# Kernel tuning notes

Hardware: AMD Instinct MI355X
Metric: run time of the kernel (lower is better)

## Reference

```python
import jax, jax.numpy as jnp
import numpy as np

ATOMF_LEN = 82
EDGE_DIM = 6
HIDDEN = 10
GNN_DEPTH = 2
N_NODES = 200000
N_EDGES = 6400000


def _lrelu(x):
    return jax.nn.leaky_relu(x, negative_slope=0.1)


def setup_inputs() -> dict:
    key = jax.random.key(0)
    ks = jax.random.split(key, 7)
    vertex = jax.random.normal(ks[0], (N_NODES, ATOMF_LEN), dtype=jnp.float32)
    edge_feat = jax.random.normal(ks[1], (N_EDGES, EDGE_DIM), dtype=jnp.float32)
    src = jax.random.randint(ks[2], (N_EDGES,), 0, N_NODES, dtype=jnp.int32)
    dst = jax.random.randint(ks[3], (N_EDGES,), 0, N_NODES, dtype=jnp.int32)
    # kaiming-uniform-ish init scale (fan_in based)
    weight_init = jax.random.uniform(ks[4], (ATOMF_LEN, HIDDEN), dtype=jnp.float32,
                                     minval=-1.0, maxval=1.0) * (np.sqrt(6.0 / ATOMF_LEN))
    gather_weight = jax.random.uniform(ks[5], (HIDDEN + EDGE_DIM, HIDDEN), dtype=jnp.float32,
                                       minval=-1.0, maxval=1.0) * (np.sqrt(6.0 / (HIDDEN + EDGE_DIM)))
    update_weight = jax.random.uniform(ks[6], (2 * HIDDEN, HIDDEN), dtype=jnp.float32,
                                       minval=-1.0, maxval=1.0) * (np.sqrt(6.0 / (2 * HIDDEN)))
    return {"vertex": vertex, "edge_feat": edge_feat, "src": src, "dst": dst,
            "weight_init": weight_init, "gather_weight": gather_weight,
            "update_weight": update_weight}


def reference(vertex, edge_feat, src, dst, weight_init, gather_weight, update_weight):
    # embedding_: leaky_relu(mm(x, W), 0.1)
    h = _lrelu(vertex @ weight_init)  # [N, HIDDEN]
    n_nodes = vertex.shape[0]
    for _ in range(GNN_DEPTH):
        # gather: per-edge message from source node hidden + edge features
        msg = _lrelu(jnp.concatenate([h[src], edge_feat], axis=1) @ gather_weight)  # [E, HIDDEN]
        # scatter-sum aggregation onto destination nodes
        agg = jax.ops.segment_sum(msg, dst, num_segments=n_nodes)  # [N, HIDDEN]
        # update: combine current hidden with aggregated messages
        h = _lrelu(jnp.concatenate([h, agg], axis=1) @ update_weight)  # [N, HIDDEN]
    return h
```

## Files before the change

### kernel.cpp

```cpp
#include <hip/hip_runtime.h>

#define ATOMF 82
#define EDGE_DIM 6
#define HIDDEN 10
#define ZPAD 16

#define BSHIFT 8
#define BUCKN (1 << BSHIFT)
#define MAXBUCK 1024
#define NB2 256
#define MAXE3 16384

__device__ __forceinline__ float lrelu(float x) { return x > 0.f ? x : 0.1f * x; }

__device__ __forceinline__ unsigned int f2bf(float f) {
    unsigned int u = __float_as_uint(f);
    return (u + 0x7fffu + ((u >> 16) & 1u)) >> 16;
}
__device__ __forceinline__ float bf2f(unsigned int b) {
    return __uint_as_float(b << 16);
}

typedef float vf2 __attribute__((ext_vector_type(2)));
__device__ __forceinline__ int nt_i(const int* p) { return __builtin_nontemporal_load(p); }
__device__ __forceinline__ vf2 nt_f2(const float* p) {
    return __builtin_nontemporal_load((const vf2*)p);
}

__global__ void embed_kernel(const float* __restrict__ vertex,
                             const float* __restrict__ W,
                             const float* __restrict__ GW,
                             float* __restrict__ h, unsigned short* __restrict__ z,
                             int n_nodes) {
    __shared__ float w[ATOMF * HIDDEN];
    __shared__ float gwh[HIDDEN * HIDDEN];
    for (int i = threadIdx.x; i < ATOMF * HIDDEN; i += blockDim.x) w[i] = W[i];
    for (int i = threadIdx.x; i < HIDDEN * HIDDEN; i += blockDim.x) gwh[i] = GW[i];
    __syncthreads();
    int node = blockIdx.x * blockDim.x + threadIdx.x;
    if (node >= n_nodes) return;
    const float2* v = (const float2*)(vertex + (long)node * ATOMF);
    float acc[HIDDEN];
#pragma unroll
    for (int j = 0; j < HIDDEN; j++) acc[j] = 0.f;
#pragma unroll 2
    for (int k2 = 0; k2 < ATOMF / 2; k2++) {
        float2 t = v[k2];
#pragma unroll
        for (int j = 0; j < HIDDEN; j++) acc[j] += t.x * w[(2 * k2) * HIDDEN + j];
#pragma unroll
        for (int j = 0; j < HIDDEN; j++) acc[j] += t.y * w[(2 * k2 + 1) * HIDDEN + j];
    }
    float ho[HIDDEN];
    float* out = h + (long)node * HIDDEN;
#pragma unroll
    for (int j = 0; j < HIDDEN; j++) { ho[j] = lrelu(acc[j]); out[j] = ho[j]; }
    float zv[HIDDEN];
#pragma unroll
    for (int j = 0; j < HIDDEN; j++) zv[j] = 0.f;
#pragma unroll
    for (int k = 0; k < HIDDEN; k++) {
        float x = ho[k];
#pragma unroll
        for (int j = 0; j < HIDDEN; j++) zv[j] += x * gwh[k * HIDDEN + j];
    }
    unsigned int* zq = (unsigned int*)(z + (size_t)node * ZPAD);
    int4 pk;
    pk.x = (int)(f2bf(zv[0]) | (f2bf(zv[1]) << 16));
    pk.y = (int)(f2bf(zv[2]) | (f2bf(zv[3]) << 16));
    pk.z = (int)(f2bf(zv[4]) | (f2bf(zv[5]) << 16));
    pk.w = (int)(f2bf(zv[6]) | (f2bf(zv[7]) << 16));
    *(int4*)zq = pk;
    zq[4] = f2bf(zv[8]) | (f2bf(zv[9]) << 16);
}

__global__ __launch_bounds__(1024) void hist_kernel(const int* __restrict__ dst,
                                                    int* __restrict__ hist,
                                                    long n_edges, int nbuck) {
    __shared__ int hl[MAXBUCK];
    for (int t = threadIdx.x; t < nbuck; t += 1024) hl[t] = 0;
    __syncthreads();
    long per = (n_edges + gridDim.x - 1) / gridDim.x;
    long s = (long)blockIdx.x * per;
    long e = s + per; if (e > n_edges) e = n_edges;
    for (long i = s + threadIdx.x; i < e; i += 1024)
        atomicAdd(&hl[nt_i(dst + i) >> BSHIFT], 1);
    __syncthreads();
    for (int t = threadIdx.x; t < nbuck; t += 1024)
        hist[(size_t)t * gridDim.x + blockIdx.x] = hl[t];
}

__global__ __launch_bounds__(1024) void scan_block_sums(const int* __restrict__ in,
                                                        int* __restrict__ partials, int n) {
    __shared__ int ws[16];
    int i = blockIdx.x * 1024 + threadIdx.x;
    int v = (i < n) ? in[i] : 0;
    int lane = threadIdx.x & 63, wid = threadIdx.x >> 6;
    int s = v;
#pragma unroll
    for (int off = 32; off > 0; off >>= 1) s += __shfl_down(s, off, 64);
    if (lane == 0) ws[wid] = s;
    __syncthreads();
    if (threadIdx.x == 0) {
        int t = 0;
#pragma unroll
        for (int k = 0; k < 16; k++) t += ws[k];
        partials[blockIdx.x] = t;
    }
}
__global__ __launch_bounds__(1024) void scan_partials(int* __restrict__ partials, int nb) {
    __shared__ int wsum[16];
    int lane = threadIdx.x & 63, wid = threadIdx.x >> 6;
    int v = (threadIdx.x < nb) ? partials[threadIdx.x] : 0;
    int incl = v;
#pragma unroll
    for (int off = 1; off < 64; off <<= 1) {
        int t = __shfl_up(incl, off, 64);
        if (lane >= off) incl += t;
    }
    if (lane == 63) wsum[wid] = incl;
    __syncthreads();
    if (wid == 0 && lane < 16) {
        int wv = wsum[lane];
        int wincl = wv;
#pragma unroll
        for (int off = 1; off < 16; off <<= 1) {
            int t = __shfl_up(wincl, off, 64);
            if (lane >= off) wincl += t;
        }
        wsum[lane] = wincl - wv;
    }
    __syncthreads();
    if (threadIdx.x < nb) partials[threadIdx.x] = wsum[wid] + (incl - v);
}
__global__ __launch_bounds__(1024) void scan_final(const int* __restrict__ in,
                                                   const int* __restrict__ partials,
                                                   int* __restrict__ out, int n) {
    __shared__ int wsum[16];
    int i = blockIdx.x * 1024 + threadIdx.x;
    int v = (i < n) ? in[i] : 0;
    int lane = threadIdx.x & 63, wid = threadIdx.x >> 6;
    int incl = v;
#pragma unroll
    for (int off = 1; off < 64; off <<= 1) {
        int t = __shfl_up(incl, off, 64);
        if (lane >= off) incl += t;
    }
    if (lane == 63) wsum[wid] = incl;
    __syncthreads();
    if (wid == 0 && lane < 16) {
        int wv = wsum[lane];
        int wincl = wv;
#pragma unroll
        for (int off = 1; off < 16; off <<= 1) {
            int t = __shfl_up(wincl, off, 64);
            if (lane >= off) wincl += t;
        }
        wsum[lane] = wincl - wv;
    }
    __syncthreads();
    if (i <= n) out[i] = partials[blockIdx.x] + wsum[wid] + (incl - v);
}

__global__ __launch_bounds__(1024) void part_scatter_kernel(
    const int* __restrict__ src, const int* __restrict__ dst,
    const float* __restrict__ ef, const int* __restrict__ base,
    int4* __restrict__ rec, long n_edges, int nbuck) {
    __shared__ int cur[MAXBUCK];
    for (int t = threadIdx.x; t < nbuck; t += 1024)
        cur[t] = base[(size_t)t * gridDim.x + blockIdx.x];
    __syncthreads();
    long per = (n_edges + gridDim.x - 1) / gridDim.x;
    long s = (long)blockIdx.x * per;
    long e = s + per; if (e > n_edges) e = n_edges;
    for (long i = s + threadIdx.x; i < e; i += 1024) {
        int d = nt_i(dst + i);
        int slot = atomicAdd(&cur[d >> BSHIFT], 1);
        const float* ep = ef + i * (long)EDGE_DIM;
        vf2 fa = nt_f2(ep), fb = nt_f2(ep + 2), fc = nt_f2(ep + 4);
        int4 r;
        r.x = nt_i(src + i) | ((d & (BUCKN - 1)) << 24);
        r.y = (int)(f2bf(fa.x) | (f2bf(fa.y) << 16));
        r.z = (int)(f2bf(fb.x) | (f2bf(fb.y) << 16));
        r.w = (int)(f2bf(fc.x) | (f2bf(fc.y) << 16));
        rec[slot] = r;
    }
}

__global__ __launch_bounds__(512) void bucket_csr_kernel(
    const int* __restrict__ base, const int4* __restrict__ rec_a, int4* __restrict__ rec_b,
    int* __restrict__ offsets, int n_nodes) {
    __shared__ unsigned char lid[MAXE3];
    __shared__ int cnt[BUCKN];
    __shared__ int excl_s[BUCKN];
    __shared__ int cursor[BUCKN];
    int b = blockIdx.x;
    int S = base[(size_t)b * NB2];
    int E = base[(size_t)(b + 1) * NB2];
    int node0 = b << BSHIFT;
    int nn = n_nodes - node0; if (nn > BUCKN) nn = BUCKN;
    if ((int)threadIdx.x < BUCKN) cnt[threadIdx.x] = 0;
    __syncthreads();
    int ne = E - S;
    bool fit = (ne <= MAXE3);
    for (int i = threadIdx.x; i < ne; i += 512) {
        int l = (int)((unsigned int)rec_a[S + i].x >> 24);
        if (fit) lid[i] = (unsigned char)l;
        atomicAdd(&cnt[l], 1);
    }
    __syncthreads();
    if (threadIdx.x == 0) {
        int run = 0;
#pragma unroll 4
        for (int l = 0; l < BUCKN; l++) { excl_s[l] = run; run += cnt[l]; }
    }
    __syncthreads();
    if ((int)threadIdx.x < nn) offsets[node0 + threadIdx.x] = S + excl_s[threadIdx.x];
    if ((int)threadIdx.x < BUCKN) cursor[threadIdx.x] = excl_s[threadIdx.x];
    if (b == (int)gridDim.x - 1 && threadIdx.x == 0) offsets[n_nodes] = E;
    __syncthreads();
    for (int i = threadIdx.x; i < ne; i += 512) {
        int4 r = rec_a[S + i];
        int l = fit ? (int)lid[i] : (int)((unsigned int)r.x >> 24);
        int q = atomicAdd(&cursor[l], 1);
        rec_b[S + q] = r;
    }
}

__global__ void count_pos_kernel(const int* __restrict__ dst, int* __restrict__ counts,
                                 unsigned short* __restrict__ pos, long n_edges) {
    long e0 = ((long)blockIdx.x * blockDim.x + threadIdx.x) * 4;
    if (e0 + 3 < n_edges) {
        int4 d = *(const int4*)(dst + e0);
        ushort4 p;
        p.x = (unsigned short)atomicAdd(&counts[d.x], 1);
        p.y = (unsigned short)atomicAdd(&counts[d.y], 1);
        p.z = (unsigned short)atomicAdd(&counts[d.z], 1);
        p.w = (unsigned short)atomicAdd(&counts[d.w], 1);
        *(ushort4*)(pos + e0) = p;
    } else {
        for (long e = e0; e < n_edges; e++)
            pos[e] = (unsigned short)atomicAdd(&counts[dst[e]], 1);
    }
}
__global__ void scatter_rec_kernel(const int* __restrict__ src, const int* __restrict__ dst,
                                   const float* __restrict__ ef,
                                   const unsigned short* __restrict__ pos,
                                   const int* __restrict__ offsets,
                                   int4* __restrict__ rec, long n_edges) {
    long e = (long)blockIdx.x * blockDim.x + threadIdx.x;
    if (e >= n_edges) return;
    int d = dst[e];
    int q = offsets[d] + (int)pos[e];
    const float2* er = (const float2*)(ef + e * (long)EDGE_DIM);
    float2 fa = er[0], fb = er[1], fc = er[2];
    int4 r;
    r.x = src[e];
    r.y = (int)(f2bf(fa.x) | (f2bf(fa.y) << 16));
    r.z = (int)(f2bf(fb.x) | (f2bf(fb.y) << 16));
    r.w = (int)(f2bf(fc.x) | (f2bf(fc.y) << 16));
    rec[q] = r;
}

__global__ __launch_bounds__(256) void gather_update_kernel(
    const float* __restrict__ h_in, const unsigned short* __restrict__ z_in,
    const int4* __restrict__ rec, const int* __restrict__ offsets,
    const float* __restrict__ GW, const float* __restrict__ UW,
    float* __restrict__ h_out, unsigned short* __restrict__ z_out,
    int n_nodes, int write_z, unsigned int src_mask) {
    __shared__ float gwh[HIDDEN * HIDDEN];
    __shared__ float gwe[EDGE_DIM * HIDDEN];
    __shared__ float uw[2 * HIDDEN * HIDDEN];
    for (int i = threadIdx.x; i < HIDDEN * HIDDEN; i += 256) gwh[i] = GW[i];
    for (int i = threadIdx.x; i < EDGE_DIM * HIDDEN; i += 256) gwe[i] = GW[HIDDEN * HIDDEN + i];
    for (int i = threadIdx.x; i < 2 * HIDDEN * HIDDEN; i += 256) uw[i] = UW[i];
    __syncthreads();
    int group = threadIdx.x >> 4;
    int sub = threadIdx.x & 15;
    int node = blockIdx.x * 16 + group;
    if (node >= n_nodes) return;
    int off0 = offsets[node], off1 = offsets[node + 1];
    float acc[HIDDEN];
#pragma unroll
    for (int j = 0; j < HIDDEN; j++) acc[j] = 0.f;
    int p = off0 + sub;
    int4 r;
    if (p < off1) r = rec[p];
    while (p < off1) {
        int pn = p + 16;
        int4 rn = r;
        if (pn < off1) rn = rec[pn];
        int sn = (int)((unsigned int)r.x & src_mask);
        const int* zq = (const int*)(z_in + (size_t)sn * ZPAD);
        int4 za = *(const int4*)zq;
        int zb = zq[4];
        float ef[EDGE_DIM];
        unsigned int u0 = (unsigned int)r.y, u1 = (unsigned int)r.z, u2 = (unsigned int)r.w;
        ef[0] = bf2f(u0 & 0xffffu); ef[1] = bf2f(u0 >> 16);
        ef[2] = bf2f(u1 & 0xffffu); ef[3] = bf2f(u1 >> 16);
        ef[4] = bf2f(u2 & 0xffffu); ef[5] = bf2f(u2 >> 16);
        float m[HIDDEN];
#pragma unroll
        for (int j = 0; j < HIDDEN; j++) m[j] = 0.f;
#pragma unroll
        for (int k = 0; k < EDGE_DIM; k++) {
            float x = ef[k];
#pragma unroll
            for (int j = 0; j < HIDDEN; j++) m[j] += x * gwe[k * HIDDEN + j];
        }
        unsigned int z0 = (unsigned int)za.x, z1 = (unsigned int)za.y;
        unsigned int z2 = (unsigned int)za.z, z3 = (unsigned int)za.w, z4 = (unsigned int)zb;
        acc[0] += lrelu(m[0] + bf2f(z0 & 0xffffu));
        acc[1] += lrelu(m[1] + bf2f(z0 >> 16));
        acc[2] += lrelu(m[2] + bf2f(z1 & 0xffffu));
        acc[3] += lrelu(m[3] + bf2f(z1 >> 16));
        acc[4] += lrelu(m[4] + bf2f(z2 & 0xffffu));
        acc[5] += lrelu(m[5] + bf2f(z2 >> 16));
        acc[6] += lrelu(m[6] + bf2f(z3 & 0xffffu));
        acc[7] += lrelu(m[7] + bf2f(z3 >> 16));
        acc[8] += lrelu(m[8] + bf2f(z4 & 0xffffu));
        acc[9] += lrelu(m[9] + bf2f(z4 >> 16));
        r = rn; p = pn;
    }
#pragma unroll
    for (int j = 0; j < HIDDEN; j++) {
#pragma unroll
        for (int d = 8; d > 0; d >>= 1) acc[j] += __shfl_down(acc[j], d, 16);
    }
    if (sub == 0) {
        float in[2 * HIDDEN];
        const float2* hp = (const float2*)(h_in + (long)node * HIDDEN);
#pragma unroll
        for (int k = 0; k < 5; k++) { float2 t = hp[k]; in[2 * k] = t.x; in[2 * k + 1] = t.y; }
#pragma unroll
        for (int j = 0; j < HIDDEN; j++) in[HIDDEN + j] = acc[j];
        float o[HIDDEN];
#pragma unroll
        for (int j = 0; j < HIDDEN; j++) o[j] = 0.f;
#pragma unroll
        for (int k = 0; k < 2 * HIDDEN; k++) {
            float x = in[k];
#pragma unroll
            for (int j = 0; j < HIDDEN; j++) o[j] += x * uw[k * HIDDEN + j];
        }
        float ho[HIDDEN];
        float* outp = h_out + (long)node * HIDDEN;
#pragma unroll
        for (int j = 0; j < HIDDEN; j++) { ho[j] = lrelu(o[j]); outp[j] = ho[j]; }
        if (write_z) {
            float zv[HIDDEN];
#pragma unroll
            for (int j = 0; j < HIDDEN; j++) zv[j] = 0.f;
#pragma unroll
            for (int k = 0; k < HIDDEN; k++) {
                float x = ho[k];
#pragma unroll
                for (int j = 0; j < HIDDEN; j++) zv[j] += x * gwh[k * HIDDEN + j];
            }
            unsigned int* zq = (unsigned int*)(z_out + (size_t)node * ZPAD);
            int4 pk;
            pk.x = (int)(f2bf(zv[0]) | (f2bf(zv[1]) << 16));
            pk.y = (int)(f2bf(zv[2]) | (f2bf(zv[3]) << 16));
            pk.z = (int)(f2bf(zv[4]) | (f2bf(zv[5]) << 16));
            pk.w = (int)(f2bf(zv[6]) | (f2bf(zv[7]) << 16));
            *(int4*)zq = pk;
            zq[4] = f2bf(zv[8]) | (f2bf(zv[9]) << 16);
        }
    }
}

extern "C" void kernel_launch(void* const* d_in, const int* in_sizes, int n_in,
                              void* d_out, int out_size, void* d_ws, size_t ws_size,
                              hipStream_t stream) {
    const float* vertex    = (const float*)d_in[0];
    const float* edge_feat = (const float*)d_in[1];
    const int*   src       = (const int*)d_in[2];
    const int*   dst       = (const int*)d_in[3];
    const float* w_init    = (const float*)d_in[4];
    const float* gw        = (const float*)d_in[5];
    const float* uw        = (const float*)d_in[6];

    const int  n_nodes = in_sizes[0] / ATOMF;
    const long n_edges = (long)in_sizes[2];
    float* out = (float*)d_out;

    const int TB = 256;
    const int node_blocks = (n_nodes + TB - 1) / TB;
    const int gu_blocks   = (n_nodes + 15) / 16;

    const int nbuck = (n_nodes + BUCKN - 1) >> BSHIFT;
    const long m = (long)nbuck * NB2;
    const int scanb_m = (int)((m + 1 + 1023) / 1024);

    size_t tbl_bytes = (size_t)n_nodes * (2 * HIDDEN * sizeof(float) + 2 * ZPAD * sizeof(unsigned short));
    size_t rec_bytes = (size_t)n_edges * sizeof(int4);

    auto al = [](size_t x) { return (x + 255) & ~(size_t)255; };
    size_t need_new = al(m * 4) + al((m + 1) * 4) + al(2048 * 4) +
                      al((size_t)(n_nodes + 1) * 4) + al(rec_bytes) +
                      al(rec_bytes > tbl_bytes ? rec_bytes : tbl_bytes);

    char* ws = (char*)d_ws;
    size_t o = 0;
    auto alloc = [&](size_t bytes) { char* p = ws + o; o = (o + bytes + 255) & ~(size_t)255; return p; };

    if (nbuck <= MAXBUCK && scanb_m <= 1024 && n_nodes <= (1 << 24) && ws_size >= need_new) {
        int*  hist     = (int*)alloc(m * 4);
        int*  base     = (int*)alloc((m + 1) * 4);
        int*  partials = (int*)alloc(2048 * 4);
        int*  offsets  = (int*)alloc((size_t)(n_nodes + 1) * 4);
        int4* rec_b    = (int4*)alloc(rec_bytes);
        char* ovl      = alloc(rec_bytes > tbl_bytes ? rec_bytes : tbl_bytes);
        int4* rec_a    = (int4*)ovl;
        float*          h0 = (float*)ovl;
        float*          h1 = h0 + (size_t)n_nodes * HIDDEN;
        unsigned short* z0 = (unsigned short*)(h1 + (size_t)n_nodes * HIDDEN);
        unsigned short* z1 = z0 + (size_t)n_nodes * ZPAD;

        hist_kernel<<<NB2, 1024, 0, stream>>>(dst, hist, n_edges, nbuck);
        scan_block_sums<<<scanb_m, 1024, 0, stream>>>(hist, partials, (int)m);
        scan_partials<<<1, 1024, 0, stream>>>(partials, scanb_m);
        scan_final<<<scanb_m, 1024, 0, stream>>>(hist, partials, base, (int)m);
        part_scatter_kernel<<<NB2, 1024, 0, stream>>>(src, dst, edge_feat, base, rec_a,
                                                      n_edges, nbuck);
        bucket_csr_kernel<<<nbuck, 512, 0, stream>>>(base, rec_a, rec_b, offsets, n_nodes);

        embed_kernel<<<node_blocks, TB, 0, stream>>>(vertex, w_init, gw, h0, z0, n_nodes);
        gather_update_kernel<<<gu_blocks, TB, 0, stream>>>(h0, z0, rec_b, offsets, gw, uw,
                                                           h1, z1, n_nodes, 1, 0x00ffffffu);
        gather_update_kernel<<<gu_blocks, TB, 0, stream>>>(h1, z1, rec_b, offsets, gw, uw,
                                                           out, z0, n_nodes, 0, 0x00ffffffu);
    } else {
        int*  counts   = (int*)alloc((size_t)(n_nodes + 1) * 4);
        int*  offsets  = (int*)alloc((size_t)(n_nodes + 1) * 4);
        int*  partials = (int*)alloc(2048 * 4);
        int4* rec      = (int4*)alloc(rec_bytes);
        size_t pos_bytes = (size_t)n_edges * sizeof(unsigned short);
        char* overlay = alloc(pos_bytes > tbl_bytes ? pos_bytes : tbl_bytes);
        unsigned short* pos = (unsigned short*)overlay;
        float*          h0  = (float*)overlay;
        float*          h1  = h0 + (size_t)n_nodes * HIDDEN;
        unsigned short* z0  = (unsigned short*)(h1 + (size_t)n_nodes * HIDDEN);
        unsigned short* z1  = z0 + (size_t)n_nodes * ZPAD;

        const int edge_blocks = (int)((n_edges + TB - 1) / TB);
        const int cp_blocks   = (int)((n_edges / 4 + TB - 1) / TB);
        const int scan_blocks = (n_nodes + 1 + 1023) / 1024;

        hipMemsetAsync(counts, 0, (size_t)(n_nodes + 1) * 4, stream);
        count_pos_kernel<<<cp_blocks, TB, 0, stream>>>(dst, counts, pos, n_edges);
        scan_block_sums<<<scan_blocks, 1024, 0, stream>>>(counts, partials, n_nodes);
        scan_partials<<<1, 1024, 0, stream>>>(partials, scan_blocks);
        scan_final<<<scan_blocks, 1024, 0, stream>>>(counts, partials, offsets, n_nodes);
        scatter_rec_kernel<<<edge_blocks, TB, 0, stream>>>(src, dst, edge_feat, pos, offsets,
                                                           rec, n_edges);
        embed_kernel<<<node_blocks, TB, 0, stream>>>(vertex, w_init, gw, h0, z0, n_nodes);
        gather_update_kernel<<<gu_blocks, TB, 0, stream>>>(h0, z0, rec, offsets, gw, uw,
                                                           h1, z1, n_nodes, 1, 0xffffffffu);
        gather_update_kernel<<<gu_blocks, TB, 0, stream>>>(h1, z1, rec, offsets, gw, uw,
                                                           out, z0, n_nodes, 0, 0xffffffffu);
    }
    (void)ws_size;
}
```

Before: 732.2 us.

## Store local bucket ids in a separate ushort array and widen buckets to 512 nodes

Local destination ids are no longer packed into the high byte of the src field. They go into a separate 16-bit side array, which bucket_csr reads in both passes in place of reloading the 16-byte records or caching ids in shared memory. Buckets grow to 512 nodes and the partition kernel uses 512 blocks, so there are half as many buckets, each with more edges. This adds 2 bytes per edge of extra write and read traffic. It also removes the src mask from the gather kernel.

```diff
diff --git a/kernel.cpp b/kernel.cpp
--- a/kernel.cpp
+++ b/kernel.cpp
@@ -5,11 +5,10 @@
 #define HIDDEN 10
 #define ZPAD 16
 
-#define BSHIFT 8
+#define BSHIFT 9
 #define BUCKN (1 << BSHIFT)
-#define MAXBUCK 1024
-#define NB2 256
-#define MAXE3 16384
+#define MAXBUCK 512
+#define NB2 512
 
 __device__ __forceinline__ float lrelu(float x) { return x > 0.f ? x : 0.1f * x; }
 
@@ -165,7 +164,8 @@
 __global__ __launch_bounds__(1024) void part_scatter_kernel(
     const int* __restrict__ src, const int* __restrict__ dst,
     const float* __restrict__ ef, const int* __restrict__ base,
-    int4* __restrict__ rec, long n_edges, int nbuck) {
+    int4* __restrict__ rec, unsigned short* __restrict__ lid16,
+    long n_edges, int nbuck) {
     __shared__ int cur[MAXBUCK];
     for (int t = threadIdx.x; t < nbuck; t += 1024)
         cur[t] = base[(size_t)t * gridDim.x + blockIdx.x];
@@ -179,18 +179,19 @@
         const float* ep = ef + i * (long)EDGE_DIM;
         vf2 fa = nt_f2(ep), fb = nt_f2(ep + 2), fc = nt_f2(ep + 4);
         int4 r;
-        r.x = nt_i(src + i) | ((d & (BUCKN - 1)) << 24);
+        r.x = nt_i(src + i);
         r.y = (int)(f2bf(fa.x) | (f2bf(fa.y) << 16));
         r.z = (int)(f2bf(fb.x) | (f2bf(fb.y) << 16));
         r.w = (int)(f2bf(fc.x) | (f2bf(fc.y) << 16));
         rec[slot] = r;
+        lid16[slot] = (unsigned short)(d & (BUCKN - 1));
     }
 }
 
 __global__ __launch_bounds__(512) void bucket_csr_kernel(
-    const int* __restrict__ base, const int4* __restrict__ rec_a, int4* __restrict__ rec_b,
+    const int* __restrict__ base, const unsigned short* __restrict__ lid16,
+    const int4* __restrict__ rec_a, int4* __restrict__ rec_b,
     int* __restrict__ offsets, int n_nodes) {
-    __shared__ unsigned char lid[MAXE3];
     __shared__ int cnt[BUCKN];
     __shared__ int excl_s[BUCKN];
     __shared__ int cursor[BUCKN];
@@ -199,15 +200,11 @@
     int E = base[(size_t)(b + 1) * NB2];
     int node0 = b << BSHIFT;
     int nn = n_nodes - node0; if (nn > BUCKN) nn = BUCKN;
-    if ((int)threadIdx.x < BUCKN) cnt[threadIdx.x] = 0;
+    cnt[threadIdx.x] = 0;
     __syncthreads();
     int ne = E - S;
-    bool fit = (ne <= MAXE3);
-    for (int i = threadIdx.x; i < ne; i += 512) {
-        int l = (int)((unsigned int)rec_a[S + i].x >> 24);
-        if (fit) lid[i] = (unsigned char)l;
-        atomicAdd(&cnt[l], 1);
-    }
+    for (int i = threadIdx.x; i < ne; i += 512)
+        atomicAdd(&cnt[lid16[S + i]], 1);
     __syncthreads();
     if (threadIdx.x == 0) {
         int run = 0;
@@ -216,12 +213,12 @@
     }
     __syncthreads();
     if ((int)threadIdx.x < nn) offsets[node0 + threadIdx.x] = S + excl_s[threadIdx.x];
-    if ((int)threadIdx.x < BUCKN) cursor[threadIdx.x] = excl_s[threadIdx.x];
+    cursor[threadIdx.x] = excl_s[threadIdx.x];
     if (b == (int)gridDim.x - 1 && threadIdx.x == 0) offsets[n_nodes] = E;
     __syncthreads();
     for (int i = threadIdx.x; i < ne; i += 512) {
         int4 r = rec_a[S + i];
-        int l = fit ? (int)lid[i] : (int)((unsigned int)r.x >> 24);
+        int l = lid16[S + i];
         int q = atomicAdd(&cursor[l], 1);
         rec_b[S + q] = r;
     }
@@ -267,7 +264,7 @@
     const int4* __restrict__ rec, const int* __restrict__ offsets,
     const float* __restrict__ GW, const float* __restrict__ UW,
     float* __restrict__ h_out, unsigned short* __restrict__ z_out,
-    int n_nodes, int write_z, unsigned int src_mask) {
+    int n_nodes, int write_z) {
     __shared__ float gwh[HIDDEN * HIDDEN];
     __shared__ float gwe[EDGE_DIM * HIDDEN];
     __shared__ float uw[2 * HIDDEN * HIDDEN];
@@ -290,8 +287,7 @@
         int pn = p + 16;
         int4 rn = r;
         if (pn < off1) rn = rec[pn];
-        int sn = (int)((unsigned int)r.x & src_mask);
-        const int* zq = (const int*)(z_in + (size_t)sn * ZPAD);
+        const int* zq = (const int*)(z_in + (size_t)(unsigned int)r.x * ZPAD);
         int4 za = *(const int4*)zq;
         int zb = zq[4];
         float ef[EDGE_DIM];
@@ -398,13 +394,14 @@
     auto al = [](size_t x) { return (x + 255) & ~(size_t)255; };
     size_t need_new = al(m * 4) + al((m + 1) * 4) + al(2048 * 4) +
                       al((size_t)(n_nodes + 1) * 4) + al(rec_bytes) +
-                      al(rec_bytes > tbl_bytes ? rec_bytes : tbl_bytes);
+                      al(rec_bytes > tbl_bytes ? rec_bytes : tbl_bytes) +
+                      al((size_t)n_edges * 2);
 
     char* ws = (char*)d_ws;
     size_t o = 0;
     auto alloc = [&](size_t bytes) { char* p = ws + o; o = (o + bytes + 255) & ~(size_t)255; return p; };
 
-    if (nbuck <= MAXBUCK && scanb_m <= 1024 && n_nodes <= (1 << 24) && ws_size >= need_new) {
+    if (nbuck <= MAXBUCK && scanb_m <= 1024 && ws_size >= need_new) {
         int*  hist     = (int*)alloc(m * 4);
         int*  base     = (int*)alloc((m + 1) * 4);
         int*  partials = (int*)alloc(2048 * 4);
@@ -412,6 +409,7 @@
         int4* rec_b    = (int4*)alloc(rec_bytes);
         char* ovl      = alloc(rec_bytes > tbl_bytes ? rec_bytes : tbl_bytes);
         int4* rec_a    = (int4*)ovl;
+        unsigned short* lid16 = (unsigned short*)alloc((size_t)n_edges * 2);
         float*          h0 = (float*)ovl;
         float*          h1 = h0 + (size_t)n_nodes * HIDDEN;
         unsigned short* z0 = (unsigned short*)(h1 + (size_t)n_nodes * HIDDEN);
@@ -422,14 +420,15 @@
         scan_partials<<<1, 1024, 0, stream>>>(partials, scanb_m);
         scan_final<<<scanb_m, 1024, 0, stream>>>(hist, partials, base, (int)m);
         part_scatter_kernel<<<NB2, 1024, 0, stream>>>(src, dst, edge_feat, base, rec_a,
-                                                      n_edges, nbuck);
-        bucket_csr_kernel<<<nbuck, 512, 0, stream>>>(base, rec_a, rec_b, offsets, n_nodes);
+                                                      lid16, n_edges, nbuck);
+        bucket_csr_kernel<<<nbuck, 512, 0, stream>>>(base, lid16, rec_a, rec_b,
+                                                     offsets, n_nodes);
 
         embed_kernel<<<node_blocks, TB, 0, stream>>>(vertex, w_init, gw, h0, z0, n_nodes);
         gather_update_kernel<<<gu_blocks, TB, 0, stream>>>(h0, z0, rec_b, offsets, gw, uw,
-                                                           h1, z1, n_nodes, 1, 0x00ffffffu);
+                                                           h1, z1, n_nodes, 1);
         gather_update_kernel<<<gu_blocks, TB, 0, stream>>>(h1, z1, rec_b, offsets, gw, uw,
-                                                           out, z0, n_nodes, 0, 0x00ffffffu);
+                                                           out, z0, n_nodes, 0);
     } else {
         int*  counts   = (int*)alloc((size_t)(n_nodes + 1) * 4);
         int*  offsets  = (int*)alloc((size_t)(n_nodes + 1) * 4);
@@ -456,9 +455,9 @@
                                                            rec, n_edges);
         embed_kernel<<<node_blocks, TB, 0, stream>>>(vertex, w_init, gw, h0, z0, n_nodes);
         gather_update_kernel<<<gu_blocks, TB, 0, stream>>>(h0, z0, rec, offsets, gw, uw,
-                                                           h1, z1, n_nodes, 1, 0xffffffffu);
+                                                           h1, z1, n_nodes, 1);
         gather_update_kernel<<<gu_blocks, TB, 0, stream>>>(h1, z1, rec, offsets, gw, uw,
-                                                           out, z0, n_nodes, 0, 0xffffffffu);
+                                                           out, z0, n_nodes, 0);
     }
     (void)ws_size;
 }
```

Result: slower. 810.1 us (+10.6%).
